# Kernel optimization log

Measured on AMD Instinct MI355X. Metric: run time of the kernel, lower is better.

Reference implementation:

```python
import jax, jax.numpy as jnp
import numpy as np

D_MODEL = 768
D_VERTEX = 32
TEMPERATURE = 1.0
ADJ_W = 0.1
SPEC_W = 0.1
EPS = 1e-8
LN_EPS = 1e-5


def _cube_buffers():
    # 64 vertices of the 6D hypercube, bit patterns (64, 6)
    bits = ((np.arange(64)[:, None] >> np.arange(6)[None, :]) & 1).astype(np.float32)
    ham = (bits[:, None, :] != bits[None, :, :]).sum(-1)
    adj = (ham == 1).astype(np.float32) * 0.5          # adjacency * 0.5 (register_cube_buffers)
    spec = 2.0 * bits - 1.0                             # (64, 6) spectral embedding
    ap = bits[:, 0]                                     # aperture subcube mask
    bd = bits[:, 1]                                     # boundary subcube mask
    rs = bits[:, 2]                                     # resonance subcube mask
    return adj, spec, ap, bd, rs


def setup_inputs() -> dict:
    key = jax.random.key(0)
    ks = jax.random.split(key, 16)
    B, S, D, DV = 2, 1024, D_MODEL, D_VERTEX
    d3 = D // 3
    x = jax.random.normal(ks[0], (B, S, D), dtype=jnp.float32)
    causal = jnp.tril(jnp.ones((S, S), dtype=jnp.float32))
    mask = jnp.broadcast_to(causal, (B, S, S))
    sc = 0.02
    Wq = jax.random.normal(ks[1], (DV, D), dtype=jnp.float32) * sc
    Wk = jax.random.normal(ks[2], (DV, D), dtype=jnp.float32) * sc
    vertex_emb = jax.random.normal(ks[3], (64, DV), dtype=jnp.float32) * sc
    vertex_gates = jax.random.normal(ks[4], (64, D), dtype=jnp.float32) * sc
    Wv = jax.random.normal(ks[5], (D, D), dtype=jnp.float32) * sc
    Wspec = jax.random.normal(ks[6], (DV, 6), dtype=jnp.float32) * sc
    Wa = jax.random.normal(ks[7], (d3, D), dtype=jnp.float32) * sc
    Wb = jax.random.normal(ks[8], (d3, D), dtype=jnp.float32) * sc
    Wr = jax.random.normal(ks[9], (D - 2 * d3, D), dtype=jnp.float32) * sc
    Wo = jax.random.normal(ks[10], (D, D), dtype=jnp.float32) * sc
    bo = jnp.zeros((D,), dtype=jnp.float32)
    gamma = jnp.ones((D,), dtype=jnp.float32)
    beta = jnp.zeros((D,), dtype=jnp.float32)
    adj, spec, ap, bd, rs = _cube_buffers()
    return {
        'x': x, 'mask': mask, 'Wq': Wq, 'Wk': Wk, 'vertex_emb': vertex_emb,
        'vertex_gates': vertex_gates, 'Wv': Wv, 'Wspec': Wspec,
        'Wa': Wa, 'Wb': Wb, 'Wr': Wr, 'Wo': Wo, 'bo': bo,
        'gamma': gamma, 'beta': beta,
        'adj_bias': jnp.asarray(adj), 'spectral_emb': jnp.asarray(spec),
        'ap_mask': jnp.asarray(ap), 'bd_mask': jnp.asarray(bd), 'rs_mask': jnp.asarray(rs),
    }


def reference(x, mask, Wq, Wk, vertex_emb, vertex_gates, Wv, Wspec, Wa, Wb, Wr,
              Wo, bo, gamma, beta, adj_bias, spectral_emb, ap_mask, bd_mask, rs_mask):
    q = x @ Wq.T                                   # (B,S,DV)
    k = x @ Wk.T                                   # (B,S,DV)
    inter = q[:, :, None, :] * k[:, None, :, :]    # (B,S,S,DV)
    # fuse vertex + spectral projections: inter@(E + sw*spec_proj).T
    spec_proj = spectral_emb @ Wspec.T             # (64, DV)
    emb = vertex_emb + SPEC_W * spec_proj          # (64, DV)
    s = jnp.einsum('bijd,vd->bijv', inter, emb)    # (B,S,S,64)
    # fuse adjacency bias: s + aw*(s@A) = s @ (I + aw*A)
    M = jnp.eye(64, dtype=s.dtype) + ADJ_W * adj_bias
    v_scores = s @ M
    pi = jax.nn.softmax(v_scores / TEMPERATURE, axis=-1)
    pi = pi * mask[..., None]

    gate_mean = jax.nn.sigmoid(vertex_gates).mean(axis=-1)   # (64,)
    scalar_attn = jnp.einsum('bijv,v->bij', pi, gate_mean)
    scalar_attn = scalar_attn / (scalar_attn.sum(-1, keepdims=True) + EPS)
    out = scalar_attn @ (x @ Wv.T)                 # (B,S,D)

    def modal(smask, W):
        mp = jnp.einsum('bijv,v->bij', pi, smask)
        mp = mp / (mp.sum(-1, keepdims=True) + EPS)
        mp = mp * mask
        mp = mp / (mp.sum(-1, keepdims=True) + EPS)
        return mp @ (x @ W.T)

    modal_out = jnp.concatenate(
        [modal(ap_mask, Wa), modal(bd_mask, Wb), modal(rs_mask, Wr)], axis=-1)
    combined = out + modal_out
    result = combined @ Wo.T + bo
    mu = result.mean(-1, keepdims=True)
    var = result.var(-1, keepdims=True)
    normed = (result - mu) * jax.lax.rsqrt(var + LN_EPS) * gamma + beta
    return normed, pi
```

## Files before the change

### kernel.cpp

```cpp
#include <hip/hip_runtime.h>

typedef unsigned short u16;
typedef unsigned int u32;
typedef __bf16 bf16x8 __attribute__((ext_vector_type(8)));
typedef float f32x4 __attribute__((ext_vector_type(4)));

#define S_LEN 1024
#define D_MODEL 768
#define N_CONV 19
#define BORROW_ROW 1888

__device__ __forceinline__ float bf2f(u16 h) {
    u32 u = ((u32)h) << 16;
    return __builtin_bit_cast(float, u);
}
__device__ __forceinline__ u16 f2bf(float f) {
    u32 u = __builtin_bit_cast(u32, f);
    u32 r = (u + 0x7fffu + ((u >> 16) & 1u)) >> 16;
    return (u16)r;
}

struct ConvArgs {
    const void* src[N_CONV];
    int n[N_CONV];
    int off[N_CONV];
};

__global__ __launch_bounds__(256) void convert_kernel(ConvArgs a, u16* __restrict__ dst,
                                                      const u16* __restrict__ probe) {
    bool isbf = (probe[0] == 0x3F80u);
    int inp = blockIdx.y;
    int n = a.n[inp];
    u16* d = dst + a.off[inp];
    const u16* s16 = (const u16*)a.src[inp];
    const float* s32 = (const float*)a.src[inp];
    int base = blockIdx.x * 1024 + threadIdx.x;
#pragma unroll
    for (int t = 0; t < 4; ++t) {
        int idx = base + t * 256;
        if (idx < n) d[idx] = isbf ? s16[idx] : f2bf(s32[idx]);
    }
}

__global__ __launch_bounds__(256) void precomp_kernel(
    const u16* __restrict__ vemb, const u16* __restrict__ vgates,
    const u16* __restrict__ Wspec, const u16* __restrict__ adj,
    const u16* __restrict__ spec, const u16* __restrict__ ap,
    const u16* __restrict__ bd, const u16* __restrict__ rs,
    u16* __restrict__ emb2bf, float* __restrict__ w4)
{
    __shared__ float emb[64 * 32];
    __shared__ float gred[256];
    int tid = threadIdx.x;
    for (int p = 0; p < 8; ++p) {
        int idx = tid + p * 256;
        int v = idx >> 5, d = idx & 31;
        float acc = bf2f(vemb[idx]);
        for (int t = 0; t < 6; ++t)
            acc += 0.1f * bf2f(spec[v * 6 + t]) * bf2f(Wspec[d * 6 + t]);
        emb[idx] = acc;
    }
    __syncthreads();
    for (int p = 0; p < 8; ++p) {
        int idx = tid + p * 256;
        int u = idx >> 5, d = idx & 31;
        float a2 = 0.f;
        for (int v = 0; v < 64; ++v)
            a2 += bf2f(adj[v * 64 + u]) * emb[v * 32 + d];
        emb2bf[idx] = f2bf(emb[idx] + 0.1f * a2);
    }
    int u = tid >> 2, qp = tid & 3;
    float acc = 0.f;
    for (int c = 0; c < 192; ++c) {
        float x = bf2f(vgates[u * 768 + qp * 192 + c]);
        acc += 1.f / (1.f + __expf(-x));
    }
    gred[tid] = acc;
    __syncthreads();
    if (qp == 0) {
        float gm = (gred[tid] + gred[tid + 1] + gred[tid + 2] + gred[tid + 3]) * (1.f / 768.f);
        w4[u * 4 + 0] = gm;
        w4[u * 4 + 1] = bf2f(ap[u]);
        w4[u * 4 + 2] = bf2f(bd[u]);
        w4[u * 4 + 3] = bf2f(rs[u]);
    }
}

template <int OUT_BF16>
__global__ __launch_bounds__(256) void gemm_abt(
    int M, int N, int K,
    const u16* __restrict__ A, long long sA,
    const u16* __restrict__ B, long long sB,
    void* __restrict__ Cout, long long sC, int ldc)
{
    int bz = blockIdx.z;
    A += (long long)bz * sA;
    B += (long long)bz * sB;
    long long cb = (long long)bz * sC;

    int lane = threadIdx.x & 63;
    int wave = threadIdx.x >> 6;
    int quad = lane >> 4, l16 = lane & 15;
    int m0 = blockIdx.x * 64 + (wave >> 1) * 32;
    int n0 = blockIdx.y * 64 + (wave & 1) * 32;

    f32x4 acc[2][2] = {};
    for (int k0 = 0; k0 < K; k0 += 32) {
        bf16x8 a[2], b[2];
#pragma unroll
        for (int mi = 0; mi < 2; ++mi) {
            int r = m0 + mi * 16 + l16;
            r = r < M ? r : M - 1;
            a[mi] = *reinterpret_cast<const bf16x8*>(A + (long long)r * K + k0 + quad * 8);
        }
#pragma unroll
        for (int ni = 0; ni < 2; ++ni) {
            int r = n0 + ni * 16 + l16;
            r = r < N ? r : N - 1;
            b[ni] = *reinterpret_cast<const bf16x8*>(B + (long long)r * K + k0 + quad * 8);
        }
#pragma unroll
        for (int mi = 0; mi < 2; ++mi)
#pragma unroll
            for (int ni = 0; ni < 2; ++ni)
                acc[mi][ni] = __builtin_amdgcn_mfma_f32_16x16x32_bf16(a[mi], b[ni], acc[mi][ni], 0, 0, 0);
    }
#pragma unroll
    for (int mi = 0; mi < 2; ++mi)
#pragma unroll
        for (int ni = 0; ni < 2; ++ni) {
            int col = n0 + ni * 16 + l16;
#pragma unroll
            for (int r = 0; r < 4; ++r) {
                int row = m0 + mi * 16 + quad * 4 + r;
                if (row < M && col < N) {
                    float v = acc[mi][ni][r];
                    if (OUT_BF16)
                        ((u16*)Cout)[cb + (long long)row * ldc + col] = f2bf(v);
                    else
                        ((float*)Cout)[cb + (long long)row * ldc + col] = v;
                }
            }
        }
}

__global__ __launch_bounds__(256) void efused_kernel(
    const u16* __restrict__ wpl, const u16* __restrict__ VX2,
    const float* __restrict__ scl, u16* __restrict__ combb)
{
    const int S = S_LEN;
    const long long SS = (long long)S * S;
    int b = blockIdx.z;
    int lane = threadIdx.x & 63;
    int wave = threadIdx.x >> 6;
    int quad = lane >> 4, l16 = lane & 15;
    int m0 = blockIdx.x * 64 + (wave >> 1) * 32;
    int n0 = blockIdx.y * 64 + (wave & 1) * 32;
    int g = (blockIdx.y * 64) >> 8;

    const u16* A0 = wpl + (long long)b * 4 * SS;
    const u16* Ag = A0 + (long long)(1 + g) * SS;
    const u16* B = VX2 + (long long)b * 1536 * S;

    f32x4 acc0[2][2] = {}, accg[2][2] = {};
    for (int k0 = 0; k0 < S; k0 += 32) {
        bf16x8 a0[2], ag[2], b0[2], bg[2];
#pragma unroll
        for (int mi = 0; mi < 2; ++mi) {
            long long r = m0 + mi * 16 + l16;
            a0[mi] = *reinterpret_cast<const bf16x8*>(A0 + r * S + k0 + quad * 8);
            ag[mi] = *reinterpret_cast<const bf16x8*>(Ag + r * S + k0 + quad * 8);
        }
#pragma unroll
        for (int ni = 0; ni < 2; ++ni) {
            long long c = n0 + ni * 16 + l16;
            b0[ni] = *reinterpret_cast<const bf16x8*>(B + c * S + k0 + quad * 8);
            bg[ni] = *reinterpret_cast<const bf16x8*>(B + (768 + c) * S + k0 + quad * 8);
        }
#pragma unroll
        for (int mi = 0; mi < 2; ++mi)
#pragma unroll
            for (int ni = 0; ni < 2; ++ni) {
                acc0[mi][ni] = __builtin_amdgcn_mfma_f32_16x16x32_bf16(a0[mi], b0[ni], acc0[mi][ni], 0, 0, 0);
                accg[mi][ni] = __builtin_amdgcn_mfma_f32_16x16x32_bf16(ag[mi], bg[ni], accg[mi][ni], 0, 0, 0);
            }
    }
    const float* s0p = scl + (long long)(b * 4) * S;
    const float* sgp = scl + (long long)(b * 4 + 1 + g) * S;
#pragma unroll
    for (int mi = 0; mi < 2; ++mi)
#pragma unroll
        for (int ni = 0; ni < 2; ++ni) {
            int col = n0 + ni * 16 + l16;
#pragma unroll
            for (int r = 0; r < 4; ++r) {
                int row = m0 + mi * 16 + quad * 4 + r;
                float v = s0p[row] * acc0[mi][ni][r] + sgp[row] * accg[mi][ni][r];
                combb[(long long)b * S * D_MODEL + (long long)row * D_MODEL + col] = f2bf(v);
            }
        }
}

template <int MODE>
__global__ __launch_bounds__(256) void stage_c_kernel(
    const float* __restrict__ qk,
    const u16* __restrict__ emb2bf,
    const float* __restrict__ w4,
    float* __restrict__ pi_out, u16* __restrict__ wpl, float* __restrict__ scales)
{
    const int S = S_LEN;
    const long long SS = (long long)S * S;
    int grow = MODE ? (BORROW_ROW + (int)blockIdx.x) : (int)blockIdx.x;
    int b = grow >> 10, i = grow & 1023;
    bool write_pi = MODE ? true : (grow < BORROW_ROW);
    int tid = threadIdx.x;
    int lane = tid & 63, wave = tid >> 6;
    int quad = lane >> 4, l16 = lane & 15;

    bf16x8 afrag[4];
#pragma unroll
    for (int mi = 0; mi < 4; ++mi)
        afrag[mi] = *reinterpret_cast<const bf16x8*>(emb2bf + (mi * 16 + l16) * 32 + quad * 8);

    const float* qp = qk + (long long)grow * 64 + quad * 8;
    f32x4 q0 = *(const f32x4*)qp;
    f32x4 q1 = *(const f32x4*)(qp + 4);

    f32x4 w4r[4][4];
    if (MODE == 0) {
#pragma unroll
        for (int mi = 0; mi < 4; ++mi)
#pragma unroll
            for (int r = 0; r < 4; ++r)
                w4r[mi][r] = *(const f32x4*)(w4 + (mi * 16 + quad * 4 + r) * 4);
    }

    float* pirow = pi_out + (long long)grow * (S * 64);
    const float* kb = qk + ((long long)(b << 10)) * 64;
    u16* wrow = wpl + (long long)(b * 4 + quad) * SS + (long long)i * S;

    float rs = 0.f;

    for (int t = wave; t < 64; t += 4) {
        int j0 = t << 4;
        int jl = j0 + l16;
        float* pdst = pirow + (long long)jl * 64 + quad * 4;
        if (j0 > i) {
            if (write_pi) {
                f32x4 z = {0.f, 0.f, 0.f, 0.f};
#pragma unroll
                for (int mi = 0; mi < 4; ++mi) *(f32x4*)(pdst + mi * 16) = z;
            }
            if (MODE == 0) wrow[jl] = 0;
            continue;
        }
        const float* kp = kb + (long long)jl * 64 + 32 + quad * 8;
        f32x4 k0 = *(const f32x4*)kp;
        f32x4 k1 = *(const f32x4*)(kp + 4);
        bf16x8 bfr;
#pragma unroll
        for (int d = 0; d < 4; ++d) bfr[d] = (__bf16)(k0[d] * q0[d]);
#pragma unroll
        for (int d = 0; d < 4; ++d) bfr[4 + d] = (__bf16)(k1[d] * q1[d]);

        f32x4 acc[4];
#pragma unroll
        for (int mi = 0; mi < 4; ++mi) {
            f32x4 z = {0.f, 0.f, 0.f, 0.f};
            acc[mi] = __builtin_amdgcn_mfma_f32_16x16x32_bf16(afrag[mi], bfr, z, 0, 0, 0);
        }
        float M = acc[0][0];
#pragma unroll
        for (int mi = 0; mi < 4; ++mi)
#pragma unroll
            for (int r = 0; r < 4; ++r) M = fmaxf(M, acc[mi][r]);
        M = fmaxf(M, __shfl_xor(M, 16));
        M = fmaxf(M, __shfl_xor(M, 32));
        float sum = 0.f;
        f32x4 pg = {0.f, 0.f, 0.f, 0.f};
        float e[4][4];
#pragma unroll
        for (int mi = 0; mi < 4; ++mi)
#pragma unroll
            for (int r = 0; r < 4; ++r) {
                float ev = __expf(acc[mi][r] - M);
                e[mi][r] = ev;
                sum += ev;
                if (MODE == 0) pg += w4r[mi][r] * ev;
            }
        sum += __shfl_xor(sum, 16);
        sum += __shfl_xor(sum, 32);
        if (MODE == 0) {
#pragma unroll
            for (int c = 0; c < 4; ++c) {
                pg[c] += __shfl_xor(pg[c], 16);
                pg[c] += __shfl_xor(pg[c], 32);
            }
        }
        float inv = 1.0f / sum;
        float sc = (jl <= i) ? inv : 0.f;
        if (write_pi) {
#pragma unroll
            for (int mi = 0; mi < 4; ++mi) {
                f32x4 pv;
#pragma unroll
                for (int r = 0; r < 4; ++r) pv[r] = e[mi][r] * sc;
                *(f32x4*)(pdst + mi * 16) = pv;
            }
        }
        if (MODE == 0) {
            float a = pg[quad] * sc;
            wrow[jl] = f2bf(a);
            rs += a;
        }
    }
    if (MODE == 1) return;
    rs += __shfl_xor(rs, 1);
    rs += __shfl_xor(rs, 2);
    rs += __shfl_xor(rs, 4);
    rs += __shfl_xor(rs, 8);
    __shared__ float sred[16];
    if (l16 == 0) sred[wave * 4 + quad] = rs;
    __syncthreads();
    if (tid < 4) {
        float R = sred[tid] + sred[4 + tid] + sred[8 + tid] + sred[12 + tid];
        float scv;
        if (tid == 0) {
            scv = 1.f / (R + 1e-8f);
        } else {
            float T1 = R + 1e-8f;
            float T2 = R / T1 + 1e-8f;
            scv = 1.f / (T1 * T2);
        }
        scales[(b * 4 + tid) * S + i] = scv;
    }
}

__global__ __launch_bounds__(256) void ln_kernel(
    const u16* __restrict__ resf, const u16* __restrict__ bo,
    const u16* __restrict__ gamma, const u16* __restrict__ beta,
    float* __restrict__ out)
{
    int row = blockIdx.x;
    int tid = threadIdx.x;
    __shared__ float red[256];
    float x[3];
#pragma unroll
    for (int p = 0; p < 3; ++p) {
        int c = tid + p * 256;
        x[p] = bf2f(resf[(long long)row * 768 + c]) + bf2f(bo[c]);
    }
    float ls = x[0] + x[1] + x[2];
    red[tid] = ls;
    __syncthreads();
    for (int st = 128; st > 0; st >>= 1) {
        if (tid < st) red[tid] += red[tid + st];
        __syncthreads();
    }
    float mu = red[0] * (1.f / 768.f);
    __syncthreads();
    float ls2 = 0.f;
#pragma unroll
    for (int p = 0; p < 3; ++p) {
        float d = x[p] - mu;
        ls2 += d * d;
    }
    red[tid] = ls2;
    __syncthreads();
    for (int st = 128; st > 0; st >>= 1) {
        if (tid < st) red[tid] += red[tid + st];
        __syncthreads();
    }
    float var = red[0] * (1.f / 768.f);
    float rstd = rsqrtf(var + 1e-5f);
#pragma unroll
    for (int p = 0; p < 3; ++p) {
        int c = tid + p * 256;
        out[(long long)row * 768 + c] = (x[p] - mu) * rstd * bf2f(gamma[c]) + bf2f(beta[c]);
    }
}

extern "C" void kernel_launch(void* const* d_in, const int* in_sizes, int n_in,
                              void* d_out, int out_size, void* d_ws, size_t ws_size,
                              hipStream_t stream)
{
    const long long S = S_LEN, D = D_MODEL, BS = 2 * S;

    float* out_norm = (float*)d_out;
    float* out_pi   = out_norm + BS * D;

    char* wsp = (char*)d_ws;
    size_t woff = 0;
    auto walloc = [&](size_t bytes) -> void* {
        void* p = wsp + woff;
        woff = (woff + bytes + 255) & ~(size_t)255;
        return p;
    };
    u16*   emb2bf = (u16*)walloc(64 * 32 * 2);
    float* w4     = (float*)walloc(64 * 4 * 4);
    float* qkbuf  = (float*)walloc(BS * 64 * 4);
    float* scl    = (float*)walloc(2 * 4 * S * 4);

    u16* borrow = (u16*)(out_pi + (long long)BORROW_ROW * S * 64);
    long long boff = 0;
    auto balloc = [&](long long elems) -> u16* {
        u16* p = borrow + boff;
        boff += (elems + 127) & ~(long long)127;
        return p;
    };

    static const int cidx[N_CONV] = {0, 2, 3, 6, 8, 9, 10, 4, 5, 7, 11, 12, 13, 14, 15, 16, 17, 18, 19};
    ConvArgs ca;
    int coff[N_CONV];
    {
        int running = 0;
        for (int t = 0; t < N_CONV; ++t) {
            ca.src[t] = d_in[cidx[t]];
            ca.n[t] = in_sizes[cidx[t]];
            coff[t] = running;
            ca.off[t] = running;
            running += (in_sizes[cidx[t]] + 127) & ~127;
        }
        (void)balloc(running);
    }
    u16* conv = borrow;
    const u16* xb      = conv + coff[0];
    const u16* Wqkb    = conv + coff[1];
    const u16* WvAllb  = conv + coff[3];
    const u16* vembb   = conv + coff[7];
    const u16* vgatesb = conv + coff[8];
    const u16* Wspecb  = conv + coff[9];
    const u16* Wob     = conv + coff[10];
    const u16* bob     = conv + coff[11];
    const u16* gammab  = conv + coff[12];
    const u16* betab   = conv + coff[13];
    const u16* adjb    = conv + coff[14];
    const u16* specb   = conv + coff[15];
    const u16* apb     = conv + coff[16];
    const u16* bdb     = conv + coff[17];
    const u16* rsb     = conv + coff[18];

    u16* VX2   = balloc(2 * 1536 * S);
    u16* combb = balloc(BS * D);
    u16* wpl   = balloc(2 * 4 * S * S);
    u16* resf  = balloc(BS * D);

    convert_kernel<<<dim3(1536, N_CONV), dim3(256), 0, stream>>>(ca, conv, (const u16*)d_in[13]);

    precomp_kernel<<<dim3(1), dim3(256), 0, stream>>>(
        vembb, vgatesb, Wspecb, adjb, specb, apb, bdb, rsb, emb2bf, w4);

    gemm_abt<0><<<dim3(32, 1, 1), 256, 0, stream>>>(
        2048, 64, 768, xb, 0, Wqkb, 0, (void*)qkbuf, 0, 64);

    gemm_abt<1><<<dim3(24, 16, 2), 256, 0, stream>>>(
        1536, 1024, 768, WvAllb, 0, xb, S * D, (void*)VX2, 1536 * S, 1024);

    stage_c_kernel<0><<<dim3(2048), dim3(256), 0, stream>>>(
        qkbuf, emb2bf, w4, out_pi, wpl, scl);

    efused_kernel<<<dim3(16, 12, 2), 256, 0, stream>>>(wpl, VX2, scl, combb);

    gemm_abt<1><<<dim3(32, 12, 1), 256, 0, stream>>>(
        2048, 768, 768, combb, 0, Wob, 0, (void*)resf, 0, 768);

    ln_kernel<<<dim3(2048), dim3(256), 0, stream>>>(resf, bob, gammab, betab, out_norm);

    stage_c_kernel<1><<<dim3(2048 - BORROW_ROW), dim3(256), 0, stream>>>(
        qkbuf, emb2bf, w4, out_pi, wpl, scl);
}
```

Measured before the change: 777.9 us.

## Fuse setup kernels, merge GEMMs, use workspace scratch, interleave stage C rows

Several changes land together. Conversion and precompute now run in one launch, and the QK and VX GEMMs share one grid. Scratch goes in the workspace when it is large enough, so the second stage_c pass that recomputed rows stored in the borrowed pi region is skipped. Stage_c blocks are ordered to pair short and long causal rows, pi is written with nontemporal stores, and the GEMM and efused loops are unrolled by 2. The risks are that the workspace path depends on ws_size, and that the GEMM bounds checks were removed.

After: 836.9 us. 1.08x slower.

```diff
diff --git a/kernel.cpp b/kernel.cpp
--- a/kernel.cpp
+++ b/kernel.cpp
@@ -18,6 +18,9 @@
     u32 u = __builtin_bit_cast(u32, f);
     u32 r = (u + 0x7fffu + ((u >> 16) & 1u)) >> 16;
     return (u16)r;
+}
+__device__ __forceinline__ float ldin(const void* p, long long i, bool isbf) {
+    return isbf ? bf2f(((const u16*)p)[i]) : ((const float*)p)[i];
 }
 
 struct ConvArgs {
@@ -26,38 +29,39 @@
     int off[N_CONV];
 };
 
-__global__ __launch_bounds__(256) void convert_kernel(ConvArgs a, u16* __restrict__ dst,
-                                                      const u16* __restrict__ probe) {
+__global__ __launch_bounds__(256) void k0_kernel(
+    ConvArgs a, u16* __restrict__ dst, const u16* __restrict__ probe,
+    const void* __restrict__ vemb, const void* __restrict__ vgates,
+    const void* __restrict__ Wspec, const void* __restrict__ adj,
+    const void* __restrict__ spec, const void* __restrict__ ap,
+    const void* __restrict__ bd, const void* __restrict__ rs,
+    u16* __restrict__ emb2bf, float* __restrict__ w4)
+{
     bool isbf = (probe[0] == 0x3F80u);
     int inp = blockIdx.y;
-    int n = a.n[inp];
-    u16* d = dst + a.off[inp];
-    const u16* s16 = (const u16*)a.src[inp];
-    const float* s32 = (const float*)a.src[inp];
-    int base = blockIdx.x * 1024 + threadIdx.x;
-#pragma unroll
-    for (int t = 0; t < 4; ++t) {
-        int idx = base + t * 256;
-        if (idx < n) d[idx] = isbf ? s16[idx] : f2bf(s32[idx]);
-    }
-}
-
-__global__ __launch_bounds__(256) void precomp_kernel(
-    const u16* __restrict__ vemb, const u16* __restrict__ vgates,
-    const u16* __restrict__ Wspec, const u16* __restrict__ adj,
-    const u16* __restrict__ spec, const u16* __restrict__ ap,
-    const u16* __restrict__ bd, const u16* __restrict__ rs,
-    u16* __restrict__ emb2bf, float* __restrict__ w4)
-{
+    if (inp < N_CONV) {
+        int n = a.n[inp];
+        u16* d = dst + a.off[inp];
+        const u16* s16 = (const u16*)a.src[inp];
+        const float* s32 = (const float*)a.src[inp];
+        int base = blockIdx.x * 1024 + threadIdx.x;
+#pragma unroll
+        for (int t = 0; t < 4; ++t) {
+            int idx = base + t * 256;
+            if (idx < n) d[idx] = isbf ? s16[idx] : f2bf(s32[idx]);
+        }
+        return;
+    }
+    if (blockIdx.x != 0) return;
     __shared__ float emb[64 * 32];
     __shared__ float gred[256];
     int tid = threadIdx.x;
     for (int p = 0; p < 8; ++p) {
         int idx = tid + p * 256;
         int v = idx >> 5, d = idx & 31;
-        float acc = bf2f(vemb[idx]);
+        float acc = ldin(vemb, idx, isbf);
         for (int t = 0; t < 6; ++t)
-            acc += 0.1f * bf2f(spec[v * 6 + t]) * bf2f(Wspec[d * 6 + t]);
+            acc += 0.1f * ldin(spec, v * 6 + t, isbf) * ldin(Wspec, d * 6 + t, isbf);
         emb[idx] = acc;
     }
     __syncthreads();
@@ -66,13 +70,13 @@
         int u = idx >> 5, d = idx & 31;
         float a2 = 0.f;
         for (int v = 0; v < 64; ++v)
-            a2 += bf2f(adj[v * 64 + u]) * emb[v * 32 + d];
+            a2 += ldin(adj, v * 64 + u, isbf) * emb[v * 32 + d];
         emb2bf[idx] = f2bf(emb[idx] + 0.1f * a2);
     }
     int u = tid >> 2, qp = tid & 3;
     float acc = 0.f;
     for (int c = 0; c < 192; ++c) {
-        float x = bf2f(vgates[u * 768 + qp * 192 + c]);
+        float x = ldin(vgates, u * 768 + qp * 192 + c, isbf);
         acc += 1.f / (1.f + __expf(-x));
     }
     gred[tid] = acc;
@@ -80,68 +84,79 @@
     if (qp == 0) {
         float gm = (gred[tid] + gred[tid + 1] + gred[tid + 2] + gred[tid + 3]) * (1.f / 768.f);
         w4[u * 4 + 0] = gm;
-        w4[u * 4 + 1] = bf2f(ap[u]);
-        w4[u * 4 + 2] = bf2f(bd[u]);
-        w4[u * 4 + 3] = bf2f(rs[u]);
-    }
-}
-
-template <int OUT_BF16>
-__global__ __launch_bounds__(256) void gemm_abt(
-    int M, int N, int K,
-    const u16* __restrict__ A, long long sA,
-    const u16* __restrict__ B, long long sB,
-    void* __restrict__ Cout, long long sC, int ldc)
-{
-    int bz = blockIdx.z;
-    A += (long long)bz * sA;
-    B += (long long)bz * sB;
-    long long cb = (long long)bz * sC;
-
+        w4[u * 4 + 1] = ldin(ap, u, isbf);
+        w4[u * 4 + 2] = ldin(bd, u, isbf);
+        w4[u * 4 + 3] = ldin(rs, u, isbf);
+    }
+}
+
+template <int KC, int OUT_BF16>
+__device__ __forceinline__ void gemm_body(
+    const u16* __restrict__ A, const u16* __restrict__ B,
+    void* __restrict__ C, int ldc, int m0, int n0, int lane)
+{
+    int quad = lane >> 4, l16 = lane & 15;
+    f32x4 acc[2][2] = {};
+#pragma unroll 2
+    for (int k0 = 0; k0 < KC; k0 += 32) {
+        bf16x8 a[2], b[2];
+#pragma unroll
+        for (int mi = 0; mi < 2; ++mi)
+            a[mi] = *reinterpret_cast<const bf16x8*>(A + (long long)(m0 + mi * 16 + l16) * KC + k0 + quad * 8);
+#pragma unroll
+        for (int ni = 0; ni < 2; ++ni)
+            b[ni] = *reinterpret_cast<const bf16x8*>(B + (long long)(n0 + ni * 16 + l16) * KC + k0 + quad * 8);
+#pragma unroll
+        for (int mi = 0; mi < 2; ++mi)
+#pragma unroll
+            for (int ni = 0; ni < 2; ++ni)
+                acc[mi][ni] = __builtin_amdgcn_mfma_f32_16x16x32_bf16(a[mi], b[ni], acc[mi][ni], 0, 0, 0);
+    }
+#pragma unroll
+    for (int mi = 0; mi < 2; ++mi)
+#pragma unroll
+        for (int ni = 0; ni < 2; ++ni) {
+            int col = n0 + ni * 16 + l16;
+#pragma unroll
+            for (int r = 0; r < 4; ++r) {
+                int row = m0 + mi * 16 + quad * 4 + r;
+                if (OUT_BF16)
+                    ((u16*)C)[(long long)row * ldc + col] = f2bf(acc[mi][ni][r]);
+                else
+                    ((float*)C)[(long long)row * ldc + col] = acc[mi][ni][r];
+            }
+        }
+}
+
+__global__ __launch_bounds__(256) void gemm_qkvx_kernel(
+    const u16* __restrict__ xb, const u16* __restrict__ Wqkb,
+    const u16* __restrict__ WvAllb, u16* __restrict__ VX2, float* __restrict__ qk)
+{
     int lane = threadIdx.x & 63;
     int wave = threadIdx.x >> 6;
-    int quad = lane >> 4, l16 = lane & 15;
+    int z = blockIdx.z;
+    if (z < 2) {
+        int m0 = blockIdx.x * 64 + (wave >> 1) * 32;
+        int n0 = blockIdx.y * 64 + (wave & 1) * 32;
+        gemm_body<768, 1>(WvAllb, xb + (long long)z * S_LEN * D_MODEL,
+                          VX2 + (long long)z * 1536 * S_LEN, S_LEN, m0, n0, lane);
+    } else {
+        int t = blockIdx.y * 24 + blockIdx.x;
+        if (t >= 32) return;
+        int m0 = t * 64 + (wave >> 1) * 32;
+        int n0 = (wave & 1) * 32;
+        gemm_body<768, 0>(xb, Wqkb, qk, 64, m0, n0, lane);
+    }
+}
+
+__global__ __launch_bounds__(256) void gemm_f_kernel(
+    const u16* __restrict__ combb, const u16* __restrict__ Wob, u16* __restrict__ resf)
+{
+    int lane = threadIdx.x & 63;
+    int wave = threadIdx.x >> 6;
     int m0 = blockIdx.x * 64 + (wave >> 1) * 32;
     int n0 = blockIdx.y * 64 + (wave & 1) * 32;
-
-    f32x4 acc[2][2] = {};
-    for (int k0 = 0; k0 < K; k0 += 32) {
-        bf16x8 a[2], b[2];
-#pragma unroll
-        for (int mi = 0; mi < 2; ++mi) {
-            int r = m0 + mi * 16 + l16;
-            r = r < M ? r : M - 1;
-            a[mi] = *reinterpret_cast<const bf16x8*>(A + (long long)r * K + k0 + quad * 8);
-        }
-#pragma unroll
-        for (int ni = 0; ni < 2; ++ni) {
-            int r = n0 + ni * 16 + l16;
-            r = r < N ? r : N - 1;
-            b[ni] = *reinterpret_cast<const bf16x8*>(B + (long long)r * K + k0 + quad * 8);
-        }
-#pragma unroll
-        for (int mi = 0; mi < 2; ++mi)
-#pragma unroll
-            for (int ni = 0; ni < 2; ++ni)
-                acc[mi][ni] = __builtin_amdgcn_mfma_f32_16x16x32_bf16(a[mi], b[ni], acc[mi][ni], 0, 0, 0);
-    }
-#pragma unroll
-    for (int mi = 0; mi < 2; ++mi)
-#pragma unroll
-        for (int ni = 0; ni < 2; ++ni) {
-            int col = n0 + ni * 16 + l16;
-#pragma unroll
-            for (int r = 0; r < 4; ++r) {
-                int row = m0 + mi * 16 + quad * 4 + r;
-                if (row < M && col < N) {
-                    float v = acc[mi][ni][r];
-                    if (OUT_BF16)
-                        ((u16*)Cout)[cb + (long long)row * ldc + col] = f2bf(v);
-                    else
-                        ((float*)Cout)[cb + (long long)row * ldc + col] = v;
-                }
-            }
-        }
+    gemm_body<768, 1>(combb, Wob, resf, 768, m0, n0, lane);
 }
 
 __global__ __launch_bounds__(256) void efused_kernel(
@@ -163,6 +178,7 @@
     const u16* B = VX2 + (long long)b * 1536 * S;
 
     f32x4 acc0[2][2] = {}, accg[2][2] = {};
+#pragma unroll 2
     for (int k0 = 0; k0 < S; k0 += 32) {
         bf16x8 a0[2], ag[2], b0[2], bg[2];
 #pragma unroll
@@ -206,13 +222,16 @@
     const float* __restrict__ qk,
     const u16* __restrict__ emb2bf,
     const float* __restrict__ w4,
-    float* __restrict__ pi_out, u16* __restrict__ wpl, float* __restrict__ scales)
+    float* __restrict__ pi_out, u16* __restrict__ wpl, float* __restrict__ scales,
+    int pi_limit)
 {
     const int S = S_LEN;
     const long long SS = (long long)S * S;
-    int grow = MODE ? (BORROW_ROW + (int)blockIdx.x) : (int)blockIdx.x;
+    int bid = blockIdx.x;
+    int g2 = bid >> 1;
+    int grow = MODE ? (BORROW_ROW + bid) : ((bid & 1) ? 2047 - g2 : g2);
     int b = grow >> 10, i = grow & 1023;
-    bool write_pi = MODE ? true : (grow < BORROW_ROW);
+    bool write_pi = MODE ? true : (grow < pi_limit);
     int tid = threadIdx.x;
     int lane = tid & 63, wave = tid >> 6;
     int quad = lane >> 4, l16 = lane & 15;
@@ -249,7 +268,8 @@
             if (write_pi) {
                 f32x4 z = {0.f, 0.f, 0.f, 0.f};
 #pragma unroll
-                for (int mi = 0; mi < 4; ++mi) *(f32x4*)(pdst + mi * 16) = z;
+                for (int mi = 0; mi < 4; ++mi)
+                    __builtin_nontemporal_store(z, (f32x4*)(pdst + mi * 16));
             }
             if (MODE == 0) wrow[jl] = 0;
             continue;
@@ -305,7 +325,7 @@
                 f32x4 pv;
 #pragma unroll
                 for (int r = 0; r < 4; ++r) pv[r] = e[mi][r] * sc;
-                *(f32x4*)(pdst + mi * 16) = pv;
+                __builtin_nontemporal_store(pv, (f32x4*)(pdst + mi * 16));
             }
         }
         if (MODE == 0) {
@@ -401,71 +421,68 @@
     float* qkbuf  = (float*)walloc(BS * 64 * 4);
     float* scl    = (float*)walloc(2 * 4 * S * 4);
 
-    u16* borrow = (u16*)(out_pi + (long long)BORROW_ROW * S * 64);
+    static const int cidx[N_CONV] = {0, 2, 3, 6, 8, 9, 10, 4, 5, 7, 11, 12, 13, 14, 15, 16, 17, 18, 19};
+    ConvArgs ca;
+    int coff[N_CONV];
+    long long conv_elems = 0;
+    for (int t = 0; t < N_CONV; ++t) {
+        ca.src[t] = d_in[cidx[t]];
+        ca.n[t] = in_sizes[cidx[t]];
+        coff[t] = (int)conv_elems;
+        ca.off[t] = (int)conv_elems;
+        conv_elems += (in_sizes[cidx[t]] + 127) & ~127;
+    }
+
+    long long bulk_elems = ((conv_elems + 127) & ~(long long)127)
+                         + 2LL * 1536 * S + 128
+                         + BS * D + 128
+                         + 2LL * 4 * S * S + 128
+                         + BS * D + 128;
+    bool usews = (ws_size >= woff + (size_t)bulk_elems * 2 + (1u << 20));
+
+    u16* bulk = usews ? (u16*)(wsp + woff)
+                      : (u16*)(out_pi + (long long)BORROW_ROW * S * 64);
     long long boff = 0;
     auto balloc = [&](long long elems) -> u16* {
-        u16* p = borrow + boff;
+        u16* p = bulk + boff;
         boff += (elems + 127) & ~(long long)127;
         return p;
     };
-
-    static const int cidx[N_CONV] = {0, 2, 3, 6, 8, 9, 10, 4, 5, 7, 11, 12, 13, 14, 15, 16, 17, 18, 19};
-    ConvArgs ca;
-    int coff[N_CONV];
-    {
-        int running = 0;
-        for (int t = 0; t < N_CONV; ++t) {
-            ca.src[t] = d_in[cidx[t]];
-            ca.n[t] = in_sizes[cidx[t]];
-            coff[t] = running;
-            ca.off[t] = running;
-            running += (in_sizes[cidx[t]] + 127) & ~127;
-        }
-        (void)balloc(running);
-    }
-    u16* conv = borrow;
+    u16* conv  = balloc(conv_elems);
+    u16* VX2   = balloc(2 * 1536 * S);
+    u16* combb = balloc(BS * D);
+    u16* wpl   = balloc(2 * 4 * S * S);
+    u16* resf  = balloc(BS * D);
+
     const u16* xb      = conv + coff[0];
     const u16* Wqkb    = conv + coff[1];
     const u16* WvAllb  = conv + coff[3];
-    const u16* vembb   = conv + coff[7];
-    const u16* vgatesb = conv + coff[8];
-    const u16* Wspecb  = conv + coff[9];
     const u16* Wob     = conv + coff[10];
     const u16* bob     = conv + coff[11];
     const u16* gammab  = conv + coff[12];
     const u16* betab   = conv + coff[13];
-    const u16* adjb    = conv + coff[14];
-    const u16* specb   = conv + coff[15];
-    const u16* apb     = conv + coff[16];
-    const u16* bdb     = conv + coff[17];
-    const u16* rsb     = conv + coff[18];
-
-    u16* VX2   = balloc(2 * 1536 * S);
-    u16* combb = balloc(BS * D);
-    u16* wpl   = balloc(2 * 4 * S * S);
-    u16* resf  = balloc(BS * D);
-
-    convert_kernel<<<dim3(1536, N_CONV), dim3(256), 0, stream>>>(ca, conv, (const u16*)d_in[13]);
-
-    precomp_kernel<<<dim3(1), dim3(256), 0, stream>>>(
-        vembb, vgatesb, Wspecb, adjb, specb, apb, bdb, rsb, emb2bf, w4);
-
-    gemm_abt<0><<<dim3(32, 1, 1), 256, 0, stream>>>(
-        2048, 64, 768, xb, 0, Wqkb, 0, (void*)qkbuf, 0, 64);
-
-    gemm_abt<1><<<dim3(24, 16, 2), 256, 0, stream>>>(
-        1536, 1024, 768, WvAllb, 0, xb, S * D, (void*)VX2, 1536 * S, 1024);
+
+    int pi_limit = usews ? 2048 : BORROW_ROW;
+
+    k0_kernel<<<dim3(1536, N_CONV + 1), dim3(256), 0, stream>>>(
+        ca, conv, (const u16*)d_in[13],
+        d_in[4], d_in[5], d_in[7], d_in[15], d_in[16], d_in[17], d_in[18], d_in[19],
+        emb2bf, w4);
+
+    gemm_qkvx_kernel<<<dim3(24, 16, 3), dim3(256), 0, stream>>>(
+        xb, Wqkb, WvAllb, VX2, qkbuf);
 
     stage_c_kernel<0><<<dim3(2048), dim3(256), 0, stream>>>(
-        qkbuf, emb2bf, w4, out_pi, wpl, scl);
-
-    efused_kernel<<<dim3(16, 12, 2), 256, 0, stream>>>(wpl, VX2, scl, combb);
-
-    gemm_abt<1><<<dim3(32, 12, 1), 256, 0, stream>>>(
-        2048, 768, 768, combb, 0, Wob, 0, (void*)resf, 0, 768);
+        qkbuf, emb2bf, w4, out_pi, wpl, scl, pi_limit);
+
+    efused_kernel<<<dim3(16, 12, 2), dim3(256), 0, stream>>>(wpl, VX2, scl, combb);
+
+    gemm_f_kernel<<<dim3(32, 12), dim3(256), 0, stream>>>(combb, Wob, resf);
 
     ln_kernel<<<dim3(2048), dim3(256), 0, stream>>>(resf, bob, gammab, betab, out_norm);
 
-    stage_c_kernel<1><<<dim3(2048 - BORROW_ROW), dim3(256), 0, stream>>>(
-        qkbuf, emb2bf, w4, out_pi, wpl, scl);
-}
+    if (!usews) {
+        stage_c_kernel<1><<<dim3(2048 - BORROW_ROW), dim3(256), 0, stream>>>(
+            qkbuf, emb2bf, w4, out_pi, wpl, scl, 2048);
+    }
+}
```
